# Kernel tuning notes

Hardware: AMD Instinct MI355X
Metric: run time of the kernel (lower is better)

## Reference

```python
import jax, jax.numpy as jnp
import numpy as np

B, T = 8, 16384
CLASSES, RC, EC = 256, 32, 256
NLAYERS = 40          # blocks(4) * layers(10)
DIL = 1024            # source uses 2**layers for every layer (faithful to code)
EPS = 1e-5


def _shift_right(x, d):
    # causal shift: y[t] = x[t-d], zero-padded
    return jnp.pad(x, ((0, 0), (0, 0), (d, 0)))[:, :, : x.shape[-1]]


def _conv1x1(x, w, b):
    # w: [out, in], x: [B, in, T]
    return jnp.einsum('oi,bit->bot', w, x) + b[None, :, None]


def _dconv2(x, w, b, d):
    # causal dilated conv, kernel 2: y[t] = w[:,:,0] x[t-d] + w[:,:,1] x[t] + b
    return (jnp.einsum('oi,bit->bot', w[:, :, 1], x)
            + jnp.einsum('oi,bit->bot', w[:, :, 0], _shift_right(x, d))
            + b[None, :, None])


def _bn(x, g, b):
    # training-mode BatchNorm1d: batch stats over (N, L)
    m = jnp.mean(x, axis=(0, 2), keepdims=True)
    v = jnp.var(x, axis=(0, 2), keepdims=True)
    return (x - m) * jax.lax.rsqrt(v + EPS) * g[None, :, None] + b[None, :, None]


def _mish(x):
    return x * jnp.tanh(jax.nn.softplus(x))


def setup_inputs() -> dict:
    key = jax.random.key(0)
    ks = jax.random.split(key, 16)
    n = jax.random.normal
    return {
        'x': n(ks[0], (B, CLASSES, T), jnp.float32),
        'start_w': n(ks[1], (RC, CLASSES), jnp.float32) * 0.05,
        'start_b': n(ks[2], (RC,), jnp.float32) * 0.05,
        'gt_w': n(ks[3], (NLAYERS, RC, RC, 2), jnp.float32) * 0.1,   # tanh branch
        'gt_b': n(ks[4], (NLAYERS, RC), jnp.float32) * 0.05,
        'gs_w': n(ks[5], (NLAYERS, RC, RC, 2), jnp.float32) * 0.1,   # sigmoid branch
        'gs_b': n(ks[6], (NLAYERS, RC), jnp.float32) * 0.05,
        'res_w': n(ks[7], (NLAYERS, RC, RC), jnp.float32) * 0.1,
        'res_b': n(ks[8], (NLAYERS, RC), jnp.float32) * 0.05,
        'bn_g': jnp.ones((NLAYERS, RC), jnp.float32),
        'bn_b': jnp.zeros((NLAYERS, RC), jnp.float32),
        'bn1_g': jnp.ones((RC,), jnp.float32),
        'bn1_b': jnp.zeros((RC,), jnp.float32),
        'e1_w': n(ks[9], (EC, RC), jnp.float32) * 0.1,
        'e1_b': n(ks[10], (EC,), jnp.float32) * 0.05,
        'bn2_g': jnp.ones((EC,), jnp.float32),
        'bn2_b': jnp.zeros((EC,), jnp.float32),
        'e2_w': n(ks[11], (CLASSES, EC), jnp.float32) * 0.05,
        'e2_b': n(ks[12], (CLASSES,), jnp.float32) * 0.05,
    }


def reference(x, start_w, start_b, gt_w, gt_b, gs_w, gs_b, res_w, res_b,
              bn_g, bn_b, bn1_g, bn1_b, e1_w, e1_b, bn2_g, bn2_b, e2_w, e2_b):
    # start_conv: CausalConv(classes, RC, k=1, shift=1) -> 1x1 conv on x shifted right by 1
    h = _conv1x1(_shift_right(x, 1), start_w, start_b)  # [B, RC, T]

    def step(carry, p):
        h, skip = carry
        gtw, gtb, gsw, gsb, rw, rb, bg, bb = p
        g = jnp.tanh(_dconv2(h, gtw, gtb, DIL)) * jax.nn.sigmoid(_dconv2(h, gsw, gsb, DIL))
        skip = skip + g
        h = h + _bn(_conv1x1(g, rw, rb), bg, bb)
        return (h, skip), None

    init = (h, jnp.zeros_like(h))
    (h, skip_sum), _ = jax.lax.scan(
        step, init, (gt_w, gt_b, gs_w, gs_b, res_w, res_b, bn_g, bn_b))

    y = _mish(_bn(skip_sum, bn1_g, bn1_b))
    y = _mish(_bn(_conv1x1(y, e1_w, e1_b), bn2_g, bn2_b))
    return _conv1x1(y, e2_w, e2_b)  # [B, CLASSES, T]
```

## Files before the change

kernel.cpp:

```cpp
#include <hip/hip_runtime.h>
#include <hip/hip_cooperative_groups.h>

namespace cg = cooperative_groups;


#define EPSV 1e-5f
#define RN   (1.f/131072.f)

#define H_OFF  0
#define SK_OFF (4*1024*1024)
#define ST_OFF (8*1024*1024)
#define ST_SKIP 2560
#define ST_MU   2624
#define ST_Y    2656
#define ST_A2   3680
#define ST_B2   3936
#define ST_TOT  4192
#define LST_N   (40*8*64)

__device__ __forceinline__ float rcp_f(float x) { return __builtin_amdgcn_rcpf(x); }
__device__ __forceinline__ float tanh_f(float x) {
    float e = __expf(2.f * x);
    return 1.f - 2.f * rcp_f(e + 1.f);
}
__device__ __forceinline__ float sigm_f(float x) { return rcp_f(1.f + __expf(-x)); }
__device__ __forceinline__ float mish_f(float x) {
    float e = __expf(x);
    float sp = (x > 15.f) ? x : __logf(1.f + e);
    return x * tanh_f(sp);
}

__global__ void k_zero(float* __restrict__ p, int n) {
    int i = blockIdx.x * 256 + threadIdx.x;
    if (i < n) p[i] = 0.f;
}

__global__ __launch_bounds__(256) void k_start(
        const float* __restrict__ x, const float* __restrict__ sw_g,
        const float* __restrict__ sb_g, float* __restrict__ h, float* __restrict__ skip)
{
    __shared__ float sw[256*36];
    __shared__ float sb[32];
    int tid = threadIdx.x, blk = blockIdx.x;
    int b = blk >> 6, r0 = (blk & 63) << 4;
    for (int k = tid; k < 8192; k += 256) {
        int o = k >> 8, c = k & 255;
        sw[c*36 + o] = sw_g[k];
    }
    if (tid < 32) sb[tid] = sb_g[tid];
    __syncthreads();

    int rr = tid & 15, s = tid >> 4;
    int t = r0 + rr + (s << 10);
    bool valid = (t >= 1);
    const float* xr = x + (long)b*256*16384 + (valid ? (t-1) : 0);
    float acc[32];
    #pragma unroll
    for (int o = 0; o < 32; ++o) acc[o] = 0.f;
    for (int c = 0; c < 256; ++c) {
        float xv = xr[(long)c*16384];
        xv = valid ? xv : 0.f;
        const float4* wrow = (const float4*)&sw[c*36];
        #pragma unroll
        for (int o4 = 0; o4 < 8; ++o4) {
            float4 w = wrow[o4];
            acc[o4*4+0] += w.x*xv; acc[o4*4+1] += w.y*xv;
            acc[o4*4+2] += w.z*xv; acc[o4*4+3] += w.w*xv;
        }
    }
    __syncthreads();
    #pragma unroll
    for (int o = 0; o < 32; ++o) sw[(rr*32 + o)*16 + s] = acc[o] + sb[o];
    __syncthreads();
    float4* hd = (float4*)(h + (long)blk*8192);
    float4* sd = (float4*)(skip + (long)blk*8192);
    const float4* ss = (const float4*)sw;
    float4 z4 = make_float4(0.f, 0.f, 0.f, 0.f);
    for (int k = tid; k < 2048; k += 256) { hd[k] = ss[k]; sd[k] = z4; }
}

__device__ __forceinline__ void stage16(float* __restrict__ row, int o,
                                        const float* __restrict__ v) {
    float4* p = (float4*)row;
    int sw = (o >> 1) & 3;
    p[0^sw] = make_float4(v[0],  v[1],  v[2],  v[3]);
    p[1^sw] = make_float4(v[4],  v[5],  v[6],  v[7]);
    p[2^sw] = make_float4(v[8],  v[9],  v[10], v[11]);
    p[3^sw] = make_float4(v[12], v[13], v[14], v[15]);
}

__device__ __forceinline__ void gate_mv(const float* __restrict__ s_w,
        const float* __restrict__ hg, int o, float gtb, float gsb,
        float* __restrict__ aT, float* __restrict__ aS)
{
    #pragma unroll
    for (int s = 0; s < 16; ++s) { aT[s] = gtb; aS[s] = gsb; }
    #pragma unroll 4
    for (int i = 0; i < 32; ++i) {
        float4 w = *(const float4*)&s_w[(i*32 + o)*4];
        const float4* hr = (const float4*)&hg[i*16];
        int swi = (i >> 1) & 3;
        float hv[16];
        *(float4*)&hv[0]  = hr[0^swi];
        *(float4*)&hv[4]  = hr[1^swi];
        *(float4*)&hv[8]  = hr[2^swi];
        *(float4*)&hv[12] = hr[3^swi];
        aT[0] += w.y*hv[0];  aS[0] += w.w*hv[0];
        #pragma unroll
        for (int s = 1; s < 16; ++s) {
            aT[s] += w.y*hv[s] + w.x*hv[s-1];
            aS[s] += w.w*hv[s] + w.z*hv[s-1];
        }
    }
}

__device__ __forceinline__ void res_mv(const float* __restrict__ s_r,
        const float* __restrict__ hg, int o, float rbv, float* __restrict__ zr)
{
    #pragma unroll
    for (int s = 0; s < 16; ++s) zr[s] = rbv;
    #pragma unroll 4
    for (int i = 0; i < 32; ++i) {
        float w = s_r[i*32 + o];
        const float4* gr = (const float4*)&hg[i*16];
        int swi = (i >> 1) & 3;
        float gv[16];
        *(float4*)&gv[0]  = gr[0^swi];
        *(float4*)&gv[4]  = gr[1^swi];
        *(float4*)&gv[8]  = gr[2^swi];
        *(float4*)&gv[12] = gr[3^swi];
        #pragma unroll
        for (int s = 0; s < 16; ++s) zr[s] += w*gv[s];
    }
}

__global__ __launch_bounds__(256, 2) void k_fused2(
        const float* __restrict__ gt_w, const float* __restrict__ gt_b,
        const float* __restrict__ gs_w, const float* __restrict__ gs_b,
        const float* __restrict__ res_w, const float* __restrict__ res_b,
        const float* __restrict__ bn_g, const float* __restrict__ bn_b,
        const float* __restrict__ h, float* __restrict__ skip,
        float* __restrict__ st, float* __restrict__ lst)
{
    __shared__ float s_w[4096];
    __shared__ float s_r[1024];
    __shared__ float s_hg[8192];
    __shared__ float s_red[4][32][2];
    __shared__ float s_ab[64];

    int tid = threadIdx.x;
    int o = tid & 31, c0 = tid >> 5;
    long baseA = (long)blockIdx.x*8192 + c0*512 + o*16;
    long baseB = baseA + 8*512;
    int slot = blockIdx.x & 7;
    float* rowA = &s_hg[c0*512 + o*16];
    float* rowB = &s_hg[(c0+8)*512 + o*16];

    float hA[16], hB[16], skA[16], skB[16], zrA[16], zrB[16];
    {
        const float4* pa = (const float4*)(h + baseA);
        const float4* pb = (const float4*)(h + baseB);
        #pragma unroll
        for (int q = 0; q < 4; ++q) {
            float4 ta = pa[q], tb = pb[q];
            hA[4*q+0]=ta.x; hA[4*q+1]=ta.y; hA[4*q+2]=ta.z; hA[4*q+3]=ta.w;
            hB[4*q+0]=tb.x; hB[4*q+1]=tb.y; hB[4*q+2]=tb.z; hB[4*q+3]=tb.w;
        }
    }
    #pragma unroll
    for (int s = 0; s < 16; ++s) { skA[s] = 0.f; skB[s] = 0.f; }

    cg::grid_group grid = cg::this_grid();

    for (int L = 0; L < 40; ++L) {
        for (int k = tid; k < 1024; k += 256) {
            int oo = k >> 5, ii = k & 31;
            float2 a = ((const float2*)(gt_w + (long)L*2048))[k];
            float2 c = ((const float2*)(gs_w + (long)L*2048))[k];
            float* d = &s_w[(ii*32 + oo)*4];
            d[0] = a.x; d[1] = a.y; d[2] = c.x; d[3] = c.y;
            s_r[ii*32 + oo] = res_w[(long)L*1024 + k];
        }
        if (L > 0 && tid < 32) {
            float ssum = 0.f, ssq = 0.f;
            #pragma unroll
            for (int r = 0; r < 8; ++r) {
                ssum += __hip_atomic_load(&lst[((L-1)*8 + r)*64 + tid],
                                          __ATOMIC_RELAXED, __HIP_MEMORY_SCOPE_AGENT);
                ssq  += __hip_atomic_load(&lst[((L-1)*8 + r)*64 + 32 + tid],
                                          __ATOMIC_RELAXED, __HIP_MEMORY_SCOPE_AGENT);
            }
            float m = ssum * RN;
            float v = ssq * RN - m*m;
            float a = rsqrtf(v + EPSV) * bn_g[(L-1)*32 + tid];
            s_ab[tid] = a;
            s_ab[32 + tid] = bn_b[(L-1)*32 + tid] - m*a;
        }
        __syncthreads();

        if (L > 0) {
            float a = s_ab[o], bb = s_ab[32 + o];
            #pragma unroll
            for (int s = 0; s < 16; ++s) {
                hA[s] += zrA[s]*a + bb;
                hB[s] += zrB[s]*a + bb;
            }
        }

        stage16(rowA, o, hA);
        stage16(rowB, o, hB);

        float gA[16], gB[16];
        {
            float aT[16], aS[16];
            float gtb = gt_b[L*32 + o], gsb = gs_b[L*32 + o];
            gate_mv(s_w, &s_hg[c0*512], o, gtb, gsb, aT, aS);
            #pragma unroll
            for (int s = 0; s < 16; ++s) {
                gA[s] = tanh_f(aT[s]) * sigm_f(aS[s]);
                skA[s] += gA[s];
            }
            gate_mv(s_w, &s_hg[(c0+8)*512], o, gtb, gsb, aT, aS);
            #pragma unroll
            for (int s = 0; s < 16; ++s) {
                gB[s] = tanh_f(aT[s]) * sigm_f(aS[s]);
                skB[s] += gB[s];
            }
        }

        if (L < 39) {
            stage16(rowA, o, gA);
            stage16(rowB, o, gB);
            float rbv = res_b[L*32 + o];
            res_mv(s_r, &s_hg[c0*512],     o, rbv, zrA);
            res_mv(s_r, &s_hg[(c0+8)*512], o, rbv, zrB);

            float ps = 0.f, pq = 0.f;
            #pragma unroll
            for (int s = 0; s < 16; ++s) {
                ps += zrA[s] + zrB[s];
                pq += zrA[s]*zrA[s] + zrB[s]*zrB[s];
            }
            ps += __shfl_down(ps, 32); pq += __shfl_down(pq, 32);
            int wv = tid >> 6;
            if ((tid & 63) < 32) { s_red[wv][o][0] = ps; s_red[wv][o][1] = pq; }
            __syncthreads();
            if (tid < 32) {
                float a = s_red[0][tid][0] + s_red[1][tid][0]
                        + s_red[2][tid][0] + s_red[3][tid][0];
                atomicAdd(&lst[(L*8 + slot)*64 + tid], a);
            } else if (tid < 64) {
                int c = tid - 32;
                float a = s_red[0][c][1] + s_red[1][c][1]
                        + s_red[2][c][1] + s_red[3][c][1];
                atomicAdd(&lst[(L*8 + slot)*64 + 32 + c], a);
            }
            grid.sync();
        }
    }

    {
        float4* pa = (float4*)(skip + baseA);
        float4* pb = (float4*)(skip + baseB);
        #pragma unroll
        for (int q = 0; q < 4; ++q) {
            pa[q] = make_float4(skA[4*q], skA[4*q+1], skA[4*q+2], skA[4*q+3]);
            pb[q] = make_float4(skB[4*q], skB[4*q+1], skB[4*q+2], skB[4*q+3]);
        }
        float p2 = 0.f, q2 = 0.f;
        #pragma unroll
        for (int s = 0; s < 16; ++s) {
            p2 += skA[s] + skB[s];
            q2 += skA[s]*skA[s] + skB[s]*skB[s];
        }
        p2 += __shfl_down(p2, 32); q2 += __shfl_down(q2, 32);
        int wv = tid >> 6;
        if ((tid & 63) < 32) { s_red[wv][o][0] = p2; s_red[wv][o][1] = q2; }
        __syncthreads();
        if (tid < 32) {
            float a = s_red[0][tid][0] + s_red[1][tid][0]
                    + s_red[2][tid][0] + s_red[3][tid][0];
            atomicAdd(&st[ST_SKIP + tid], a);
        } else if (tid < 64) {
            int c = tid - 32;
            float a = s_red[0][c][1] + s_red[1][c][1]
                    + s_red[2][c][1] + s_red[3][c][1];
            atomicAdd(&st[ST_SKIP + 32 + c], a);
        }
    }
}

__global__ __launch_bounds__(256) void k_layer(
        const float* __restrict__ gt_w, const float* __restrict__ gt_b,
        const float* __restrict__ gs_w, const float* __restrict__ gs_b,
        const float* __restrict__ res_w, const float* __restrict__ res_b,
        const float* __restrict__ bn_g, const float* __restrict__ bn_b,
        float* __restrict__ h, float* __restrict__ z, float* __restrict__ skip,
        float* __restrict__ st, int L)
{
    __shared__ float s_w[4096];
    __shared__ float s_r[1024];
    __shared__ float s_hg[4096];
    __shared__ float s_red[4][32][2];

    int tid = threadIdx.x;
    int o = tid & 31, chl = tid >> 5;
    long base = (long)blockIdx.x*4096 + chl*512 + o*16;

    for (int k = tid; k < 1024; k += 256) {
        int oo = k >> 5, ii = k & 31;
        float2 a = ((const float2*)(gt_w + (long)L*2048))[k];
        float2 c = ((const float2*)(gs_w + (long)L*2048))[k];
        float* d = &s_w[(ii*32 + oo)*4];
        d[0] = a.x; d[1] = a.y; d[2] = c.x; d[3] = c.y;
        s_r[ii*32 + oo] = res_w[(long)L*1024 + k];
    }

    float hreg[16];
    float4* hp4 = (float4*)(h + base);
    #pragma unroll
    for (int q = 0; q < 4; ++q) {
        float4 t4 = hp4[q];
        hreg[4*q+0]=t4.x; hreg[4*q+1]=t4.y; hreg[4*q+2]=t4.z; hreg[4*q+3]=t4.w;
    }
    if (L > 0) {
        float ssum = st[(L-1)*64 + o], ssq = st[(L-1)*64 + 32 + o];
        float m = ssum * RN;
        float v = ssq * RN - m*m;
        float a = rsqrtf(v + EPSV) * bn_g[(L-1)*32 + o];
        float bb = bn_b[(L-1)*32 + o] - m*a;
        const float4* zp4 = (const float4*)(z + base);
        #pragma unroll
        for (int q = 0; q < 4; ++q) {
            float4 t4 = zp4[q];
            hreg[4*q+0] += t4.x*a + bb; hreg[4*q+1] += t4.y*a + bb;
            hreg[4*q+2] += t4.z*a + bb; hreg[4*q+3] += t4.w*a + bb;
        }
        #pragma unroll
        for (int q = 0; q < 4; ++q)
            hp4[q] = make_float4(hreg[4*q], hreg[4*q+1], hreg[4*q+2], hreg[4*q+3]);
    }
    float4* hs4 = (float4*)&s_hg[chl*512 + o*16];
    #pragma unroll
    for (int q = 0; q < 4; ++q)
        hs4[q] = make_float4(hreg[4*q], hreg[4*q+1], hreg[4*q+2], hreg[4*q+3]);
    __syncthreads();

    float aT[16], aS[16];
    float gtb = gt_b[L*32 + o], gsb = gs_b[L*32 + o];
    #pragma unroll
    for (int s = 0; s < 16; ++s) { aT[s] = gtb; aS[s] = gsb; }
    #pragma unroll 4
    for (int i = 0; i < 32; ++i) {
        float4 w = *(const float4*)&s_w[(i*32 + o)*4];
        const float4* hr = (const float4*)&s_hg[chl*512 + i*16];
        float hp = 0.f;
        #pragma unroll
        for (int s4 = 0; s4 < 4; ++s4) {
            float4 hv = hr[s4];
            int s = 4*s4;
            aT[s+0] += w.y*hv.x + w.x*hp;   aS[s+0] += w.w*hv.x + w.z*hp;
            aT[s+1] += w.y*hv.y + w.x*hv.x; aS[s+1] += w.w*hv.y + w.z*hv.x;
            aT[s+2] += w.y*hv.z + w.x*hv.y; aS[s+2] += w.w*hv.z + w.z*hv.y;
            aT[s+3] += w.y*hv.w + w.x*hv.z; aS[s+3] += w.w*hv.w + w.z*hv.z;
            hp = hv.w;
        }
    }
    float g[16], sk[16];
    #pragma unroll
    for (int s = 0; s < 16; ++s) g[s] = tanh_f(aT[s]) * sigm_f(aS[s]);

    float4* skp4 = (float4*)(skip + base);
    #pragma unroll
    for (int q = 0; q < 4; ++q) {
        float4 t4 = skp4[q];
        sk[4*q+0] = t4.x + g[4*q+0]; sk[4*q+1] = t4.y + g[4*q+1];
        sk[4*q+2] = t4.z + g[4*q+2]; sk[4*q+3] = t4.w + g[4*q+3];
        skp4[q] = make_float4(sk[4*q], sk[4*q+1], sk[4*q+2], sk[4*q+3]);
    }

    __syncthreads();
    #pragma unroll
    for (int q = 0; q < 4; ++q)
        hs4[q] = make_float4(g[4*q], g[4*q+1], g[4*q+2], g[4*q+3]);
    __syncthreads();

    float az[16];
    float rbv = res_b[L*32 + o];
    #pragma unroll
    for (int s = 0; s < 16; ++s) az[s] = rbv;
    #pragma unroll 4
    for (int i = 0; i < 32; ++i) {
        float w = s_r[i*32 + o];
        const float4* gr = (const float4*)&s_hg[chl*512 + i*16];
        #pragma unroll
        for (int s4 = 0; s4 < 4; ++s4) {
            float4 gv = gr[s4];
            az[4*s4+0] += w*gv.x; az[4*s4+1] += w*gv.y;
            az[4*s4+2] += w*gv.z; az[4*s4+3] += w*gv.w;
        }
    }
    float4* zp4w = (float4*)(z + base);
    #pragma unroll
    for (int q = 0; q < 4; ++q)
        zp4w[q] = make_float4(az[4*q], az[4*q+1], az[4*q+2], az[4*q+3]);

    float ps = 0.f, pq = 0.f;
    #pragma unroll
    for (int s = 0; s < 16; ++s) { ps += az[s]; pq += az[s]*az[s]; }
    ps += __shfl_down(ps, 32); pq += __shfl_down(pq, 32);
    int wv = tid >> 6;
    if ((tid & 63) < 32) { s_red[wv][o][0] = ps; s_red[wv][o][1] = pq; }
    __syncthreads();
    if (tid < 32) {
        float a = s_red[0][tid][0] + s_red[1][tid][0] + s_red[2][tid][0] + s_red[3][tid][0];
        atomicAdd(&st[L*64 + tid], a);
    } else if (tid < 64) {
        int c = tid - 32;
        float a = s_red[0][c][1] + s_red[1][c][1] + s_red[2][c][1] + s_red[3][c][1];
        atomicAdd(&st[L*64 + 32 + c], a);
    }

    if (L == 39) {
        float p2 = 0.f, q2 = 0.f;
        #pragma unroll
        for (int s = 0; s < 16; ++s) { p2 += sk[s]; q2 += sk[s]*sk[s]; }
        p2 += __shfl_down(p2, 32); q2 += __shfl_down(q2, 32);
        __syncthreads();
        if ((tid & 63) < 32) { s_red[wv][o][0] = p2; s_red[wv][o][1] = q2; }
        __syncthreads();
        if (tid < 32) {
            float a = s_red[0][tid][0] + s_red[1][tid][0] + s_red[2][tid][0] + s_red[3][tid][0];
            atomicAdd(&st[ST_SKIP + tid], a);
        } else if (tid < 64) {
            int c = tid - 32;
            float a = s_red[0][c][1] + s_red[1][c][1] + s_red[2][c][1] + s_red[3][c][1];
            atomicAdd(&st[ST_SKIP + 32 + c], a);
        }
    }
}

__global__ __launch_bounds__(256) void k_ep_a(
        const float* __restrict__ skip, const float* __restrict__ bn1_g,
        const float* __restrict__ bn1_b, float* __restrict__ st)
{
    __shared__ float sy[256*33];
    __shared__ float sA[32], sB[32];
    int tid = threadIdx.x;
    long cb = (long)blockIdx.x * 8192;
    if (tid < 32) {
        float ssum = st[ST_SKIP + tid], ssq = st[ST_SKIP + 32 + tid];
        float m = ssum * RN, v = ssq * RN - m*m;
        float a = rsqrtf(v + EPSV) * bn1_g[tid];
        sA[tid] = a; sB[tid] = bn1_b[tid] - m*a;
    }
    __syncthreads();
    for (int k = tid; k < 8192; k += 256) {
        int i = k & 31, p = k >> 5;
        int rr = p & 15, s = p >> 4;
        float v = skip[cb + rr*512 + i*16 + s];
        sy[p*33 + i] = mish_f(v * sA[i] + sB[i]);
    }
    __syncthreads();
    if (tid < 32) {
        float mu = 0.f;
        for (int p = 0; p < 256; ++p) mu += sy[p*33 + tid];
        atomicAdd(&st[ST_MU + tid], mu);
    }
    int jj = tid & 31, i0 = tid >> 5;
    float a0 = 0.f, a1 = 0.f, a2 = 0.f, a3 = 0.f;
    for (int p = 0; p < 256; ++p) {
        float yj = sy[p*33 + jj];
        a0 += yj * sy[p*33 + i0];
        a1 += yj * sy[p*33 + i0 + 8];
        a2 += yj * sy[p*33 + i0 + 16];
        a3 += yj * sy[p*33 + i0 + 24];
    }
    atomicAdd(&st[ST_Y + (i0     )*32 + jj], a0);
    atomicAdd(&st[ST_Y + (i0 +  8)*32 + jj], a1);
    atomicAdd(&st[ST_Y + (i0 + 16)*32 + jj], a2);
    atomicAdd(&st[ST_Y + (i0 + 24)*32 + jj], a3);
}

__global__ void k_ep_b(
        const float* __restrict__ e1_w, const float* __restrict__ e1_b,
        const float* __restrict__ bn2_g, const float* __restrict__ bn2_b,
        float* __restrict__ st)
{
    __shared__ float mu[32];
    int o = threadIdx.x;
    if (o < 32) mu[o] = st[ST_MU + o] * RN;
    __syncthreads();
    float w[32];
    const float4* wr = (const float4*)(e1_w + o*32);
    #pragma unroll
    for (int q = 0; q < 8; ++q) {
        float4 t4 = wr[q];
        w[4*q]=t4.x; w[4*q+1]=t4.y; w[4*q+2]=t4.z; w[4*q+3]=t4.w;
    }
    float m2 = e1_b[o];
    #pragma unroll
    for (int i = 0; i < 32; ++i) m2 += w[i]*mu[i];
    float var = 0.f;
    for (int i = 0; i < 32; ++i) {
        float wi = w[i], mi = mu[i];
        for (int j = 0; j < 32; ++j)
            var += wi * w[j] * (st[ST_Y + i*32 + j]*RN - mi*mu[j]);
    }
    float a2 = rsqrtf(var + EPSV) * bn2_g[o];
    st[ST_A2 + o] = a2;
    st[ST_B2 + o] = bn2_b[o] - m2*a2;
}

__global__ __launch_bounds__(256, 4) void k_ep_c(
        const float* __restrict__ skip,
        const float* __restrict__ bn1_g, const float* __restrict__ bn1_b,
        const float* __restrict__ e1_w, const float* __restrict__ e1_b,
        const float* __restrict__ e2_w, const float* __restrict__ e2_b,
        const float* __restrict__ st, float* __restrict__ out)
{
    __shared__ float y1l[32*32];
    __shared__ float y2l[256*36];
    int tid = threadIdx.x;
    int blk2 = blockIdx.x;
    int blk = blk2 >> 1, half = blk2 & 1;
    int b = blk >> 6, r0 = (blk & 63) << 4;
    long cb = (long)blk * 8192;
    float w1[32];
    {
        const float4* wr = (const float4*)(e1_w + tid*32);
        #pragma unroll
        for (int q = 0; q < 8; ++q) {
            float4 t4 = wr[q];
            w1[4*q]=t4.x; w1[4*q+1]=t4.y; w1[4*q+2]=t4.z; w1[4*q+3]=t4.w;
        }
    }
    float a2 = st[ST_A2 + tid], b2 = st[ST_B2 + tid];
    float eb1 = e1_b[tid];
    float eb2 = e2_b[tid];
    const float4* w2row = (const float4*)(e2_w + (long)tid * 256);

    for (int st8 = half*4; st8 < half*4 + 4; ++st8) {
        for (int k = tid; k < 1024; k += 256) {
            int i = k >> 5, q = k & 31;
            float ssum = st[ST_SKIP + i], ssq = st[ST_SKIP + 32 + i];
            float m = ssum * RN, vv = ssq * RN - m*m;
            float a1 = rsqrtf(vv + EPSV) * bn1_g[i];
            float b1 = bn1_b[i] - m*a1;
            int rr = q & 15, sl = q >> 4;
            float v = skip[cb + rr*512 + i*16 + st8*2 + sl];
            y1l[i*32 + q] = mish_f(v * a1 + b1);
        }
        __syncthreads();
        #pragma unroll 2
        for (int q4 = 0; q4 < 8; ++q4) {
            float4 acc = make_float4(eb1, eb1, eb1, eb1);
            #pragma unroll 8
            for (int i = 0; i < 32; ++i) {
                float4 yv = *(const float4*)&y1l[i*32 + q4*4];
                float wi = w1[i];
                acc.x += wi*yv.x; acc.y += wi*yv.y; acc.z += wi*yv.z; acc.w += wi*yv.w;
            }
            float4 y2v;
            y2v.x = mish_f(acc.x*a2 + b2);
            y2v.y = mish_f(acc.y*a2 + b2);
            y2v.z = mish_f(acc.z*a2 + b2);
            y2v.w = mish_f(acc.w*a2 + b2);
            *(float4*)&y2l[tid*36 + q4*4] = y2v;
        }
        __syncthreads();
        float acc[32];
        #pragma unroll
        for (int q = 0; q < 32; ++q) acc[q] = eb2;
        for (int i4 = 0; i4 < 64; ++i4) {
            float4 w4 = w2row[i4];
            float wa[4] = {w4.x, w4.y, w4.z, w4.w};
            #pragma unroll
            for (int ii = 0; ii < 4; ++ii) {
                float wv = wa[ii];
                const float* yr = &y2l[(i4*4 + ii)*36];
                #pragma unroll
                for (int q4 = 0; q4 < 8; ++q4) {
                    float4 yv = *(const float4*)&yr[q4*4];
                    acc[q4*4+0] += wv*yv.x; acc[q4*4+1] += wv*yv.y;
                    acc[q4*4+2] += wv*yv.z; acc[q4*4+3] += wv*yv.w;
                }
            }
        }
        long ob = ((long)b*256 + tid)*16384 + (long)(st8*2)*1024 + r0;
        float4* op = (float4*)&out[ob];
        op[0] = make_float4(acc[0],  acc[1],  acc[2],  acc[3]);
        op[1] = make_float4(acc[4],  acc[5],  acc[6],  acc[7]);
        op[2] = make_float4(acc[8],  acc[9],  acc[10], acc[11]);
        op[3] = make_float4(acc[12], acc[13], acc[14], acc[15]);
        float4* op2 = (float4*)&out[ob + 1024];
        op2[0] = make_float4(acc[16], acc[17], acc[18], acc[19]);
        op2[1] = make_float4(acc[20], acc[21], acc[22], acc[23]);
        op2[2] = make_float4(acc[24], acc[25], acc[26], acc[27]);
        op2[3] = make_float4(acc[28], acc[29], acc[30], acc[31]);
    }
}

extern "C" void kernel_launch(void* const* d_in, const int* in_sizes, int n_in,
                              void* d_out, int out_size, void* d_ws, size_t ws_size,
                              hipStream_t stream) {
    const float* x       = (const float*)d_in[0];
    const float* start_w = (const float*)d_in[1];
    const float* start_b = (const float*)d_in[2];
    const float* gt_w    = (const float*)d_in[3];
    const float* gt_b    = (const float*)d_in[4];
    const float* gs_w    = (const float*)d_in[5];
    const float* gs_b    = (const float*)d_in[6];
    const float* res_w   = (const float*)d_in[7];
    const float* res_b   = (const float*)d_in[8];
    const float* bn_g    = (const float*)d_in[9];
    const float* bn_b    = (const float*)d_in[10];
    const float* bn1_g   = (const float*)d_in[11];
    const float* bn1_b   = (const float*)d_in[12];
    const float* e1_w    = (const float*)d_in[13];
    const float* e1_b    = (const float*)d_in[14];
    const float* bn2_g   = (const float*)d_in[15];
    const float* bn2_b   = (const float*)d_in[16];
    const float* e2_w    = (const float*)d_in[17];
    const float* e2_b    = (const float*)d_in[18];
    float* ws  = (float*)d_ws;
    float* out = (float*)d_out;

    float* h    = ws + H_OFF;
    float* skip = ws + SK_OFF;
    float* st   = ws + ST_OFF;
    float* lst  = out;

    int coop_ok = 0;
    {
        int dev = 0, attr = 0, occ = 0;
        if (hipGetDevice(&dev) == hipSuccess &&
            hipDeviceGetAttribute(&attr, hipDeviceAttributeCooperativeLaunch, dev)
                == hipSuccess && attr) {
            if (hipOccupancyMaxActiveBlocksPerMultiprocessor(&occ, k_fused2, 256, 0)
                    == hipSuccess && occ >= 2)
                coop_ok = 1;
        }
    }

    k_zero<<<dim3(17), dim3(256), 0, stream>>>(st, ST_TOT);
    k_zero<<<dim3(80), dim3(256), 0, stream>>>(lst, LST_N);
    k_start<<<dim3(512), dim3(256), 0, stream>>>(x, start_w, start_b, h, skip);

    if (coop_ok) {
        void* kargs[12] = {
            (void*)&gt_w, (void*)&gt_b, (void*)&gs_w, (void*)&gs_b,
            (void*)&res_w, (void*)&res_b, (void*)&bn_g, (void*)&bn_b,
            (void*)&h, (void*)&skip, (void*)&st, (void*)&lst };
        if (hipLaunchCooperativeKernel(k_fused2, dim3(512), dim3(256),
                                       kargs, 0, stream) != hipSuccess)
            coop_ok = 0;
    }
    if (!coop_ok) {
        size_t need_full = ((size_t)ST_OFF + 8192 + 4*1024*1024) * 4;
        float* z = (ws_size >= need_full) ? (ws + ST_OFF + 8192)
                                          : (float*)d_out;
        for (int L = 0; L < 40; ++L)
            k_layer<<<dim3(1024), dim3(256), 0, stream>>>(
                gt_w, gt_b, gs_w, gs_b, res_w, res_b, bn_g, bn_b, h, z, skip, st, L);
    }

    k_ep_a<<<dim3(512), dim3(256), 0, stream>>>(skip, bn1_g, bn1_b, st);
    k_ep_b<<<dim3(1), dim3(256), 0, stream>>>(e1_w, e1_b, bn2_g, bn2_b, st);
    k_ep_c<<<dim3(1024), dim3(256), 0, stream>>>(skip, bn1_g, bn1_b, e1_w, e1_b,
                                                 e2_w, e2_b, st, out);
}
```

Before: 2.595 ms.

## Split persistent cooperative kernel into 1024 smaller blocks for higher occupancy

```diff
diff --git a/kernel.cpp b/kernel.cpp
--- a/kernel.cpp
+++ b/kernel.cpp
@@ -16,7 +16,9 @@
 #define ST_A2   3680
 #define ST_B2   3936
 #define ST_TOT  4192
-#define LST_N   (40*8*64)
+#define NSLOT  16
+#define LST_N  (40*NSLOT*64)
+#define NBLK   1024
 
 __device__ __forceinline__ float rcp_f(float x) { return __builtin_amdgcn_rcpf(x); }
 __device__ __forceinline__ float tanh_f(float x) {
@@ -134,7 +136,7 @@
     }
 }
 
-__global__ __launch_bounds__(256, 2) void k_fused2(
+__global__ __launch_bounds__(256, 4) void k_fused3(
         const float* __restrict__ gt_w, const float* __restrict__ gt_b,
         const float* __restrict__ gs_w, const float* __restrict__ gs_b,
         const float* __restrict__ res_w, const float* __restrict__ res_b,
@@ -144,31 +146,27 @@
 {
     __shared__ float s_w[4096];
     __shared__ float s_r[1024];
-    __shared__ float s_hg[8192];
+    __shared__ float s_hg[4096];
     __shared__ float s_red[4][32][2];
     __shared__ float s_ab[64];
 
     int tid = threadIdx.x;
-    int o = tid & 31, c0 = tid >> 5;
-    long baseA = (long)blockIdx.x*8192 + c0*512 + o*16;
-    long baseB = baseA + 8*512;
-    int slot = blockIdx.x & 7;
-    float* rowA = &s_hg[c0*512 + o*16];
-    float* rowB = &s_hg[(c0+8)*512 + o*16];
-
-    float hA[16], hB[16], skA[16], skB[16], zrA[16], zrB[16];
+    int o = tid & 31, chl = tid >> 5;
+    long base = (long)blockIdx.x*4096 + chl*512 + o*16;
+    int slot = blockIdx.x & (NSLOT-1);
+    float* row = &s_hg[chl*512 + o*16];
+
+    float hreg[16], sk[16], zr[16];
     {
-        const float4* pa = (const float4*)(h + baseA);
-        const float4* pb = (const float4*)(h + baseB);
+        const float4* pa = (const float4*)(h + base);
         #pragma unroll
         for (int q = 0; q < 4; ++q) {
-            float4 ta = pa[q], tb = pb[q];
-            hA[4*q+0]=ta.x; hA[4*q+1]=ta.y; hA[4*q+2]=ta.z; hA[4*q+3]=ta.w;
-            hB[4*q+0]=tb.x; hB[4*q+1]=tb.y; hB[4*q+2]=tb.z; hB[4*q+3]=tb.w;
-        }
-    }
-    #pragma unroll
-    for (int s = 0; s < 16; ++s) { skA[s] = 0.f; skB[s] = 0.f; }
+            float4 t4 = pa[q];
+            hreg[4*q+0]=t4.x; hreg[4*q+1]=t4.y; hreg[4*q+2]=t4.z; hreg[4*q+3]=t4.w;
+        }
+    }
+    #pragma unroll
+    for (int s = 0; s < 16; ++s) sk[s] = 0.f;
 
     cg::grid_group grid = cg::this_grid();
 
@@ -184,10 +182,10 @@
         if (L > 0 && tid < 32) {
             float ssum = 0.f, ssq = 0.f;
             #pragma unroll
-            for (int r = 0; r < 8; ++r) {
-                ssum += __hip_atomic_load(&lst[((L-1)*8 + r)*64 + tid],
+            for (int r = 0; r < NSLOT; ++r) {
+                ssum += __hip_atomic_load(&lst[((L-1)*NSLOT + r)*64 + tid],
                                           __ATOMIC_RELAXED, __HIP_MEMORY_SCOPE_AGENT);
-                ssq  += __hip_atomic_load(&lst[((L-1)*8 + r)*64 + 32 + tid],
+                ssq  += __hip_atomic_load(&lst[((L-1)*NSLOT + r)*64 + 32 + tid],
                                           __ATOMIC_RELAXED, __HIP_MEMORY_SCOPE_AGENT);
             }
             float m = ssum * RN;
@@ -201,46 +199,29 @@
         if (L > 0) {
             float a = s_ab[o], bb = s_ab[32 + o];
             #pragma unroll
-            for (int s = 0; s < 16; ++s) {
-                hA[s] += zrA[s]*a + bb;
-                hB[s] += zrB[s]*a + bb;
-            }
-        }
-
-        stage16(rowA, o, hA);
-        stage16(rowB, o, hB);
-
-        float gA[16], gB[16];
+            for (int s = 0; s < 16; ++s) hreg[s] += zr[s]*a + bb;
+        }
+
+        stage16(row, o, hreg);
+
+        float g[16];
         {
             float aT[16], aS[16];
-            float gtb = gt_b[L*32 + o], gsb = gs_b[L*32 + o];
-            gate_mv(s_w, &s_hg[c0*512], o, gtb, gsb, aT, aS);
+            gate_mv(s_w, &s_hg[chl*512], o, gt_b[L*32 + o], gs_b[L*32 + o], aT, aS);
             #pragma unroll
             for (int s = 0; s < 16; ++s) {
-                gA[s] = tanh_f(aT[s]) * sigm_f(aS[s]);
-                skA[s] += gA[s];
+                g[s] = tanh_f(aT[s]) * sigm_f(aS[s]);
+                sk[s] += g[s];
             }
-            gate_mv(s_w, &s_hg[(c0+8)*512], o, gtb, gsb, aT, aS);
-            #pragma unroll
-            for (int s = 0; s < 16; ++s) {
-                gB[s] = tanh_f(aT[s]) * sigm_f(aS[s]);
-                skB[s] += gB[s];
-            }
         }
 
         if (L < 39) {
-            stage16(rowA, o, gA);
-            stage16(rowB, o, gB);
-            float rbv = res_b[L*32 + o];
-            res_mv(s_r, &s_hg[c0*512],     o, rbv, zrA);
-            res_mv(s_r, &s_hg[(c0+8)*512], o, rbv, zrB);
+            stage16(row, o, g);
+            res_mv(s_r, &s_hg[chl*512], o, res_b[L*32 + o], zr);
 
             float ps = 0.f, pq = 0.f;
             #pragma unroll
-            for (int s = 0; s < 16; ++s) {
-                ps += zrA[s] + zrB[s];
-                pq += zrA[s]*zrA[s] + zrB[s]*zrB[s];
-            }
+            for (int s = 0; s < 16; ++s) { ps += zr[s]; pq += zr[s]*zr[s]; }
             ps += __shfl_down(ps, 32); pq += __shfl_down(pq, 32);
             int wv = tid >> 6;
             if ((tid & 63) < 32) { s_red[wv][o][0] = ps; s_red[wv][o][1] = pq; }
@@ -248,33 +229,29 @@
             if (tid < 32) {
                 float a = s_red[0][tid][0] + s_red[1][tid][0]
                         + s_red[2][tid][0] + s_red[3][tid][0];
-                atomicAdd(&lst[(L*8 + slot)*64 + tid], a);
+                atomicAdd(&lst[(L*NSLOT + slot)*64 + tid], a);
             } else if (tid < 64) {
                 int c = tid - 32;
                 float a = s_red[0][c][1] + s_red[1][c][1]
                         + s_red[2][c][1] + s_red[3][c][1];
-                atomicAdd(&lst[(L*8 + slot)*64 + 32 + c], a);
+                atomicAdd(&lst[(L*NSLOT + slot)*64 + 32 + c], a);
             }
             grid.sync();
         }
     }
 
     {
-        float4* pa = (float4*)(skip + baseA);
-        float4* pb = (float4*)(skip + baseB);
-        #pragma unroll
-        for (int q = 0; q < 4; ++q) {
-            pa[q] = make_float4(skA[4*q], skA[4*q+1], skA[4*q+2], skA[4*q+3]);
-            pb[q] = make_float4(skB[4*q], skB[4*q+1], skB[4*q+2], skB[4*q+3]);
-        }
+        float4* pa = (float4*)(skip + base);
+        #pragma unroll
+        for (int q = 0; q < 4; ++q)
+            pa[q] = make_float4(sk[4*q], sk[4*q+1], sk[4*q+2], sk[4*q+3]);
+
         float p2 = 0.f, q2 = 0.f;
         #pragma unroll
-        for (int s = 0; s < 16; ++s) {
-            p2 += skA[s] + skB[s];
-            q2 += skA[s]*skA[s] + skB[s]*skB[s];
-        }
+        for (int s = 0; s < 16; ++s) { p2 += sk[s]; q2 += sk[s]*sk[s]; }
         p2 += __shfl_down(p2, 32); q2 += __shfl_down(q2, 32);
         int wv = tid >> 6;
+        __syncthreads();
         if ((tid & 63) < 32) { s_red[wv][o][0] = p2; s_red[wv][o][1] = q2; }
         __syncthreads();
         if (tid < 32) {
@@ -637,14 +614,14 @@
         if (hipGetDevice(&dev) == hipSuccess &&
             hipDeviceGetAttribute(&attr, hipDeviceAttributeCooperativeLaunch, dev)
                 == hipSuccess && attr) {
-            if (hipOccupancyMaxActiveBlocksPerMultiprocessor(&occ, k_fused2, 256, 0)
-                    == hipSuccess && occ >= 2)
+            if (hipOccupancyMaxActiveBlocksPerMultiprocessor(&occ, k_fused3, 256, 0)
+                    == hipSuccess && occ >= 4)
                 coop_ok = 1;
         }
     }
 
     k_zero<<<dim3(17), dim3(256), 0, stream>>>(st, ST_TOT);
-    k_zero<<<dim3(80), dim3(256), 0, stream>>>(lst, LST_N);
+    k_zero<<<dim3(160), dim3(256), 0, stream>>>(lst, LST_N);
     k_start<<<dim3(512), dim3(256), 0, stream>>>(x, start_w, start_b, h, skip);
 
     if (coop_ok) {
@@ -652,7 +629,7 @@
             (void*)&gt_w, (void*)&gt_b, (void*)&gs_w, (void*)&gs_b,
             (void*)&res_w, (void*)&res_b, (void*)&bn_g, (void*)&bn_b,
             (void*)&h, (void*)&skip, (void*)&st, (void*)&lst };
-        if (hipLaunchCooperativeKernel(k_fused2, dim3(512), dim3(256),
+        if (hipLaunchCooperativeKernel(k_fused3, dim3(NBLK), dim3(256),
                                        kargs, 0, stream) != hipSuccess)
             coop_ok = 0;
     }
```

Result: no change. 2.623 ms (+1.1%).
